# Performance work log

Measured on AMD Instinct MI355X. Metric: run time of the kernel, lower is better.

The kernel has to match this reference:

```python
import jax, jax.numpy as jnp
import numpy as np

HEADS = 8
HEAD_DIM = 32
PRE_H = 32
PRE_W = 32
SCALE = HEAD_DIM ** (-0.5)


def _relative_indices(H, W):
    # Faithful to torch loop: out[p, q] = (gy[q]-y_p+H)*W + (gx[q]-x_p+W)
    gy, gx = np.meshgrid(np.arange(H), np.arange(W), indexing='ij')
    gy = gy.reshape(-1)
    gx = gx.reshape(-1)
    idx = (gy[None, :] - gy[:, None] + H) * W + (gx[None, :] - gx[:, None] + W)
    return idx.astype(np.int32)  # [HW, HW]


def setup_inputs() -> dict:
    key = jax.random.key(0)
    ks = jax.random.split(key, 7)
    b, c, H, W = 16, 256, PRE_H, PRE_W
    dim = HEADS * HEAD_DIM  # 256
    x = jax.random.normal(ks[0], (b, c, H, W), dtype=jnp.float32)
    # nn.Linear weights: [out_features, in_features]
    Wq = jax.random.normal(ks[1], (dim, c), dtype=jnp.float32) * 0.02
    Wk = jax.random.normal(ks[2], (dim, c), dtype=jnp.float32) * 0.02
    Wv = jax.random.normal(ks[3], (dim, c), dtype=jnp.float32) * 0.02
    Wo = jax.random.normal(ks[4], (c, dim), dtype=jnp.float32) * 0.02
    bo = jax.random.normal(ks[5], (c,), dtype=jnp.float32) * 0.02
    rel_bias = jax.random.normal(ks[6], (HEADS, (2 * PRE_H - 1) * (2 * PRE_W - 1)), dtype=jnp.float32)
    rel_idx = jnp.asarray(_relative_indices(PRE_H, PRE_W))
    return {"x": x, "Wq": Wq, "Wk": Wk, "Wv": Wv, "Wo": Wo, "bo": bo,
            "rel_bias": rel_bias, "rel_idx": rel_idx}


def reference(x, Wq, Wk, Wv, Wo, bo, rel_bias, rel_idx):
    b, c, H, W = x.shape
    n = H * W
    h, d = HEADS, HEAD_DIM
    # b c h w -> b (h w) c
    xt = x.reshape(b, c, n).transpose(0, 2, 1)
    q = (xt @ Wq.T).reshape(b, n, h, d).transpose(0, 2, 1, 3)  # b h n d
    k = (xt @ Wk.T).reshape(b, n, h, d).transpose(0, 2, 1, 3)
    v = (xt @ Wv.T).reshape(b, n, h, d).transpose(0, 2, 1, 3)
    k = k * SCALE
    # gathered relative bias: [h, n, n]
    bias = rel_bias[:, rel_idx]
    attn = jnp.einsum('bhnd,bhmd->bhnm', q, k) + bias[None]
    attn = jax.nn.softmax(attn, axis=-1)
    out = jnp.einsum('bhnm,bhmd->bhnd', attn, v)
    out = out.transpose(0, 2, 1, 3).reshape(b, n, h * d)  # b n (h d)
    out = out @ Wo.T + bo
    # b (h w) c -> b c h w
    return out.transpose(0, 2, 1).reshape(b, c, H, W)
```

## Files before the change

kernel.cpp:

```cpp
#include <hip/hip_runtime.h>

#define HEADS 8
#define HDIM 32
#define NTOK 1024
#define CDIM 256
#define BATCH 16
#define ATT_SCALE 0.17677669529663687f
#define L2E 1.4426950408889634f
#define BSTR 1544

typedef __attribute__((ext_vector_type(8))) short bf16x8;
typedef __attribute__((ext_vector_type(4))) float f32x4;

__device__ __forceinline__ unsigned short f2bf(float f) {
    unsigned int u = __float_as_uint(f);
    return (unsigned short)((u + 0x7fffu + ((u >> 16) & 1u)) >> 16);
}

__device__ __forceinline__ unsigned cvt_pk_bf16(float lo, float hi) {
    unsigned r;
    asm("v_cvt_pk_bf16_f32 %0, %1, %2" : "=v"(r) : "v"(lo), "v"(hi));
    return r;
}

__global__ __launch_bounds__(256) void prep_kernel(
    const float* __restrict__ x,
    const float* __restrict__ Wq, const float* __restrict__ Wk,
    const float* __restrict__ Wv, const float* __restrict__ Wo,
    unsigned short* __restrict__ w16, unsigned short* __restrict__ xt16)
{
    const int t = threadIdx.x;
    if (blockIdx.z == 16) {
        const int which = blockIdx.y;
        const float* src = (which == 0) ? Wq : ((which == 1) ? Wk : ((which == 2) ? Wv : Wo));
        const float scale = (which == 1) ? (ATT_SCALE * L2E) : 1.0f;
        const int base = (blockIdx.x * 256 + t) * 16;
        #pragma unroll
        for (int i = 0; i < 4; ++i) {
            const int idx = base + i * 4;
            float4 v = *(const float4*)&src[idx];
            union { unsigned short h[4]; uint2 u; } pk;
            pk.h[0] = f2bf(v.x * scale); pk.h[1] = f2bf(v.y * scale);
            pk.h[2] = f2bf(v.z * scale); pk.h[3] = f2bf(v.w * scale);
            *(uint2*)&w16[(size_t)which * 65536 + idx] = pk.u;
        }
        return;
    }
    __shared__ float tile[64][65];
    const int b = blockIdx.z, ct = blockIdx.y * 64, nt = blockIdx.x * 64;
    const float* xb = x + ((size_t)b * CDIM + ct) * NTOK + nt;
    const int cc = t >> 4, n4 = (t & 15) * 4;
    #pragma unroll
    for (int i = 0; i < 4; ++i) {
        float4 v = *(const float4*)&xb[(size_t)(cc + 16 * i) * NTOK + n4];
        tile[cc + 16 * i][n4]     = v.x;
        tile[cc + 16 * i][n4 + 1] = v.y;
        tile[cc + 16 * i][n4 + 2] = v.z;
        tile[cc + 16 * i][n4 + 3] = v.w;
    }
    __syncthreads();
    const int c0 = (t & 7) * 8;
    #pragma unroll
    for (int i = 0; i < 2; ++i) {
        const int nl = (t >> 3) + 32 * i;
        union { unsigned short h[8]; uint4 u; } pk;
        #pragma unroll
        for (int j = 0; j < 8; ++j) pk.h[j] = f2bf(tile[c0 + j][nl]);
        *(uint4*)&xt16[((size_t)b * NTOK + nt + nl) * CDIM + ct + c0] = pk.u;
    }
}

__global__ __launch_bounds__(1024, 4) void attn_kernel(
    const unsigned short* __restrict__ xt16,
    const unsigned short* __restrict__ w16,
    const float* __restrict__ rel_bias,
    unsigned short* __restrict__ ao16)
{
    __shared__ __align__(16) unsigned char smem[65536 + 65536 + BSTR * 4 * 4];
    unsigned short* k_s   = (unsigned short*)smem;
    unsigned short* v_s   = (unsigned short*)(smem + 65536);
    unsigned short* q_s   = (unsigned short*)(smem + 65536);
    float*          bias4 = (float*)(smem + 131072);

    const int id   = blockIdx.x;
    const int bh_i = (id & 7) * 16 + (id >> 4);
    const int half = (id >> 3) & 1;
    const int b = bh_i >> 3, h = bh_i & 7;

    const int t = threadIdx.x, wid = t >> 6, lane = t & 63;
    const int g = lane >> 4, ln = lane & 15;
    const int qb = half * 512 + wid * 32;

    const unsigned short* xb  = xt16 + (size_t)b * NTOK * CDIM;
    const unsigned short* wqh = w16 + (size_t)(h * 32) * CDIM;
    const unsigned short* wkh = w16 + 65536 + (size_t)(h * 32) * CDIM;
    const unsigned short* wvh = w16 + 2 * 65536 + (size_t)(h * 32) * CDIM;

    {
        const int START = 544 - 512 * half;
        const float* brow = rel_bias + (size_t)h * 3969;
        for (int i = t; i < 1540; i += 1024) {
            #pragma unroll
            for (int a = 0; a < 4; ++a)
                bias4[a * BSTR + i] = brow[START + a + i] * L2E;
        }
    }

    bf16x8 aq0, aq1;
    {
        f32x4 acc[2][2];
        #pragma unroll
        for (int m = 0; m < 2; ++m)
            #pragma unroll
            for (int n = 0; n < 2; ++n) acc[m][n] = (f32x4){0.f, 0.f, 0.f, 0.f};
        #pragma unroll
        for (int kt = 0; kt < CDIM; kt += 32) {
            bf16x8 a[2], w2[2];
            #pragma unroll
            for (int m = 0; m < 2; ++m)
                a[m] = *(const bf16x8*)&xb[(size_t)(qb + m * 16 + ln) * CDIM + kt + g * 8];
            #pragma unroll
            for (int n = 0; n < 2; ++n)
                w2[n] = *(const bf16x8*)&wqh[(size_t)(n * 16 + ln) * CDIM + kt + g * 8];
            #pragma unroll
            for (int m = 0; m < 2; ++m)
                #pragma unroll
                for (int n = 0; n < 2; ++n)
                    acc[m][n] = __builtin_amdgcn_mfma_f32_16x16x32_bf16(a[m], w2[n], acc[m][n], 0, 0, 0);
        }
        const int lr = wid * 32;
        #pragma unroll
        for (int m = 0; m < 2; ++m)
            #pragma unroll
            for (int n = 0; n < 2; ++n)
                #pragma unroll
                for (int r = 0; r < 4; ++r)
                    q_s[(size_t)(lr + m * 16 + g * 4 + r) * HDIM + n * 16 + ln] = f2bf(acc[m][n][r]);
        aq0 = *(const bf16x8*)&q_s[(size_t)(lr + ln) * HDIM + g * 8];
        aq1 = *(const bf16x8*)&q_s[(size_t)(lr + 16 + ln) * HDIM + g * 8];
    }

    __syncthreads();

    {
        const int tr = wid * 64;
        f32x4 ak[4][2], av[2][4];
        #pragma unroll
        for (int m = 0; m < 4; ++m)
            #pragma unroll
            for (int n = 0; n < 2; ++n) {
                ak[m][n] = (f32x4){0.f, 0.f, 0.f, 0.f};
                av[n][m] = (f32x4){0.f, 0.f, 0.f, 0.f};
            }
        #pragma unroll
        for (int kt = 0; kt < CDIM; kt += 32) {
            bf16x8 xf[4], wkf[2], wvf[2];
            #pragma unroll
            for (int m = 0; m < 4; ++m)
                xf[m] = *(const bf16x8*)&xb[(size_t)(tr + m * 16 + ln) * CDIM + kt + g * 8];
            #pragma unroll
            for (int n = 0; n < 2; ++n) {
                wkf[n] = *(const bf16x8*)&wkh[(size_t)(n * 16 + ln) * CDIM + kt + g * 8];
                wvf[n] = *(const bf16x8*)&wvh[(size_t)(n * 16 + ln) * CDIM + kt + g * 8];
            }
            #pragma unroll
            for (int m = 0; m < 4; ++m) {
                ak[m][0] = __builtin_amdgcn_mfma_f32_16x16x32_bf16(xf[m], wkf[0], ak[m][0], 0, 0, 0);
                ak[m][1] = __builtin_amdgcn_mfma_f32_16x16x32_bf16(xf[m], wkf[1], ak[m][1], 0, 0, 0);
                av[0][m] = __builtin_amdgcn_mfma_f32_16x16x32_bf16(wvf[0], xf[m], av[0][m], 0, 0, 0);
                av[1][m] = __builtin_amdgcn_mfma_f32_16x16x32_bf16(wvf[1], xf[m], av[1][m], 0, 0, 0);
            }
        }
        #pragma unroll
        for (int m = 0; m < 4; ++m) {
            const int fbase = (2 * wid + (m >> 1)) * 2 + (g & 1);
            #pragma unroll
            for (int n = 0; n < 2; ++n) {
                const int lhi = (2 * n + (ln >> 3)) * 16 + ((m & 1) * 2 + (g >> 1)) * 4;
                #pragma unroll
                for (int r = 0; r < 4; ++r)
                    k_s[fbase * 512 + (lhi + r) * 8 + (ln & 7)] = f2bf(ak[m][n][r]);
            }
        }
        #pragma unroll
        for (int n = 0; n < 2; ++n)
            #pragma unroll
            for (int m = 0; m < 4; ++m) {
                const int fr  = (2 * wid + (m >> 1)) * 2 + n;
                const int lnb = ((m & 1) * 2 + (ln >> 3)) * 16 + g * 4;
                #pragma unroll
                for (int r = 0; r < 4; ++r)
                    v_s[fr * 512 + (lnb + r) * 8 + (ln & 7)] = f2bf(av[n][m][r]);
            }
    }

    __syncthreads();

    const int boffL = 512 + 8 * g - wid * 32 - ln;
    const int ba = boffL & 3;
    const float* bb = &bias4[ba * BSTR + (boffL - ba)];
    const unsigned short* kfp = k_s + lane * 8;
    const unsigned short* vfp = v_s + lane * 8;

    f32x4 o00 = {0.f,0.f,0.f,0.f}, o01 = {0.f,0.f,0.f,0.f};
    f32x4 o10 = {0.f,0.f,0.f,0.f}, o11 = {0.f,0.f,0.f,0.f};
    f32x4 ls0 = {0.f,0.f,0.f,0.f}, ls1 = {0.f,0.f,0.f,0.f};
    const short one_bf = (short)0x3F80;
    const bf16x8 ones = {one_bf,one_bf,one_bf,one_bf,one_bf,one_bf,one_bf,one_bf};

    bf16x8 kf0 = *(const bf16x8*)&kfp[0];
    bf16x8 kf1 = *(const bf16x8*)&kfp[512];
    f32x4  cA0 = *(const f32x4*)&bb[0];
    f32x4  cA1 = *(const f32x4*)&bb[4];
    f32x4  cB0 = *(const f32x4*)&bb[-16];
    f32x4  cB1 = *(const f32x4*)&bb[-12];

    for (int kb = 0; kb < NTOK; kb += 32) {
        const int fi = (kb >> 5) * 2;
        const bf16x8 vA0 = *(const bf16x8*)&vfp[fi * 512];
        const bf16x8 vA1 = *(const bf16x8*)&vfp[(fi + 1) * 512];
        const int kn = (kb + 32) & (NTOK - 1);
        const int fn = (kn >> 5) * 2;
        const bf16x8 nk0 = *(const bf16x8*)&kfp[fn * 512];
        const bf16x8 nk1 = *(const bf16x8*)&kfp[(fn + 1) * 512];
        const f32x4  nA0 = *(const f32x4*)&bb[kn];
        const f32x4  nA1 = *(const f32x4*)&bb[kn + 4];
        const f32x4  nB0 = *(const f32x4*)&bb[kn - 16];
        const f32x4  nB1 = *(const f32x4*)&bb[kn - 12];

        __builtin_amdgcn_s_setprio(1);
        f32x4 s00 = __builtin_amdgcn_mfma_f32_16x16x32_bf16(kf0, aq0, cA0, 0, 0, 0);
        f32x4 s01 = __builtin_amdgcn_mfma_f32_16x16x32_bf16(kf1, aq0, cA1, 0, 0, 0);
        f32x4 s10 = __builtin_amdgcn_mfma_f32_16x16x32_bf16(kf0, aq1, cB0, 0, 0, 0);
        f32x4 s11 = __builtin_amdgcn_mfma_f32_16x16x32_bf16(kf1, aq1, cB1, 0, 0, 0);
        __builtin_amdgcn_s_setprio(0);

        union { unsigned u4[4]; bf16x8 v; } ap0, ap1;
        ap0.u4[0] = cvt_pk_bf16(__builtin_amdgcn_exp2f(s00[0]), __builtin_amdgcn_exp2f(s00[1]));
        ap0.u4[1] = cvt_pk_bf16(__builtin_amdgcn_exp2f(s00[2]), __builtin_amdgcn_exp2f(s00[3]));
        ap0.u4[2] = cvt_pk_bf16(__builtin_amdgcn_exp2f(s01[0]), __builtin_amdgcn_exp2f(s01[1]));
        ap0.u4[3] = cvt_pk_bf16(__builtin_amdgcn_exp2f(s01[2]), __builtin_amdgcn_exp2f(s01[3]));
        ap1.u4[0] = cvt_pk_bf16(__builtin_amdgcn_exp2f(s10[0]), __builtin_amdgcn_exp2f(s10[1]));
        ap1.u4[1] = cvt_pk_bf16(__builtin_amdgcn_exp2f(s10[2]), __builtin_amdgcn_exp2f(s10[3]));
        ap1.u4[2] = cvt_pk_bf16(__builtin_amdgcn_exp2f(s11[0]), __builtin_amdgcn_exp2f(s11[1]));
        ap1.u4[3] = cvt_pk_bf16(__builtin_amdgcn_exp2f(s11[2]), __builtin_amdgcn_exp2f(s11[3]));

        __builtin_amdgcn_s_setprio(1);
        o00 = __builtin_amdgcn_mfma_f32_16x16x32_bf16(ap0.v, vA0, o00, 0, 0, 0);
        o01 = __builtin_amdgcn_mfma_f32_16x16x32_bf16(ap0.v, vA1, o01, 0, 0, 0);
        ls0 = __builtin_amdgcn_mfma_f32_16x16x32_bf16(ap0.v, ones, ls0, 0, 0, 0);
        o10 = __builtin_amdgcn_mfma_f32_16x16x32_bf16(ap1.v, vA0, o10, 0, 0, 0);
        o11 = __builtin_amdgcn_mfma_f32_16x16x32_bf16(ap1.v, vA1, o11, 0, 0, 0);
        ls1 = __builtin_amdgcn_mfma_f32_16x16x32_bf16(ap1.v, ones, ls1, 0, 0, 0);
        __builtin_amdgcn_s_setprio(0);

        kf0 = nk0; kf1 = nk1;
        cA0 = nA0; cA1 = nA1; cB0 = nB0; cB1 = nB1;
    }

    #pragma unroll
    for (int r = 0; r < 4; ++r) {
        float i0 = 1.f / ls0[r], i1 = 1.f / ls1[r];
        o00[r] *= i0; o01[r] *= i0;
        o10[r] *= i1; o11[r] *= i1;
    }

    __syncthreads();
    unsigned short (*otr)[32][40] = (unsigned short(*)[32][40])smem;
    #pragma unroll
    for (int r = 0; r < 4; ++r) {
        otr[wid][g * 4 + r][ln]           = f2bf(o00[r]);
        otr[wid][g * 4 + r][16 + ln]      = f2bf(o01[r]);
        otr[wid][16 + g * 4 + r][ln]      = f2bf(o10[r]);
        otr[wid][16 + g * 4 + r][16 + ln] = f2bf(o11[r]);
    }
    const int row = lane >> 1;
    const int ch  = (lane & 1) * 16;
    uint4 st0 = *(uint4*)&otr[wid][row][ch];
    uint4 st1 = *(uint4*)&otr[wid][row][ch + 8];
    unsigned short* dst = &ao16[((size_t)b * NTOK + qb + row) * CDIM + h * HDIM + ch];
    *(uint4*)dst     = st0;
    *(uint4*)&dst[8] = st1;
}

__global__ __launch_bounds__(256) void outproj_kernel(
    const unsigned short* __restrict__ ao16,
    const unsigned short* __restrict__ wo16,
    const float* __restrict__ bo,
    float* __restrict__ y)
{
    const int id   = blockIdx.x;
    const int b    = (id & 7) * 2 + ((id >> 3) & 1);
    const int rest = id >> 4;
    const int ct   = (rest & 3) * 64;
    const int pt   = (rest >> 2) * 128;
    const int t = threadIdx.x, wid = t >> 6, lane = t & 63;
    const int g = lane >> 4, ln = lane & 15;
    const int cb2 = ct + (wid & 1) * 32;
    const int pb  = pt + (wid >> 1) * 64;
    const unsigned short* ab = ao16 + (size_t)b * NTOK * CDIM;

    f32x4 acc[2][4];
    #pragma unroll
    for (int n = 0; n < 2; ++n)
        #pragma unroll
        for (int m = 0; m < 4; ++m) acc[n][m] = (f32x4){0.f, 0.f, 0.f, 0.f};

    #pragma unroll
    for (int kt = 0; kt < CDIM; kt += 32) {
        bf16x8 aw[2], bx[4];
        #pragma unroll
        for (int n = 0; n < 2; ++n)
            aw[n] = *(const bf16x8*)&wo16[(size_t)(cb2 + n * 16 + ln) * CDIM + kt + g * 8];
        #pragma unroll
        for (int m = 0; m < 4; ++m)
            bx[m] = *(const bf16x8*)&ab[(size_t)(pb + m * 16 + ln) * CDIM + kt + g * 8];
        #pragma unroll
        for (int n = 0; n < 2; ++n)
            #pragma unroll
            for (int m = 0; m < 4; ++m)
                acc[n][m] = __builtin_amdgcn_mfma_f32_16x16x32_bf16(aw[n], bx[m], acc[n][m], 0, 0, 0);
    }
    #pragma unroll
    for (int n = 0; n < 2; ++n)
        #pragma unroll
        for (int r = 0; r < 4; ++r) {
            const int c = cb2 + n * 16 + g * 4 + r;
            const float bias = bo[c];
            #pragma unroll
            for (int m = 0; m < 4; ++m)
                y[((size_t)b * CDIM + c) * NTOK + pb + m * 16 + ln] = acc[n][m][r] + bias;
        }
}

extern "C" void kernel_launch(void* const* d_in, const int* in_sizes, int n_in,
                              void* d_out, int out_size, void* d_ws, size_t ws_size,
                              hipStream_t stream) {
    const float* x        = (const float*)d_in[0];
    const float* Wq       = (const float*)d_in[1];
    const float* Wk       = (const float*)d_in[2];
    const float* Wv       = (const float*)d_in[3];
    const float* Wo       = (const float*)d_in[4];
    const float* bo       = (const float*)d_in[5];
    const float* rel_bias = (const float*)d_in[6];
    (void)in_sizes; (void)n_in; (void)ws_size; (void)out_size;

    unsigned short* ws16 = (unsigned short*)d_ws;
    unsigned short* xt16 = ws16;
    unsigned short* ao16 = ws16 + (size_t)4 * 1024 * 1024;
    unsigned short* w16  = ws16 + (size_t)8 * 1024 * 1024;
    float* y = (float*)d_out;

    prep_kernel<<<dim3(16, 4, 17), 256, 0, stream>>>(x, Wq, Wk, Wv, Wo, w16, xt16);
    attn_kernel<<<256, 1024, 0, stream>>>(xt16, w16, rel_bias, ao16);
    outproj_kernel<<<512, 256, 0, stream>>>(ao16, w16 + 3 * 65536, bo, y);
}
```

Before: 168.4 us.

## Fuse prep, attention and output projection into one cooperative persistent kernel

Merges the three kernels (bf16 conversion and transpose, attention, output projection) into a single cooperative kernel of 256 blocks of 1024 threads, separated by grid-wide syncs. This removes two kernel launch boundaries and the tail gaps between them. In exchange, the output projection and prep phases now run with the attention kernel's large shared-memory and register footprint and only 256 blocks. Grid syncs add their own barrier overhead and need every block to be co-resident.

```diff
diff --git a/kernel.cpp b/kernel.cpp
--- a/kernel.cpp
+++ b/kernel.cpp
@@ -1,4 +1,7 @@
 #include <hip/hip_runtime.h>
+#include <hip/hip_cooperative_groups.h>
+
+namespace cg = cooperative_groups;
 
 #define HEADS 8
 #define HDIM 32
@@ -23,314 +26,319 @@
     return r;
 }
 
-__global__ __launch_bounds__(256) void prep_kernel(
+__global__ __launch_bounds__(1024, 4) void fused_kernel(
     const float* __restrict__ x,
     const float* __restrict__ Wq, const float* __restrict__ Wk,
     const float* __restrict__ Wv, const float* __restrict__ Wo,
-    unsigned short* __restrict__ w16, unsigned short* __restrict__ xt16)
-{
-    const int t = threadIdx.x;
-    if (blockIdx.z == 16) {
-        const int which = blockIdx.y;
-        const float* src = (which == 0) ? Wq : ((which == 1) ? Wk : ((which == 2) ? Wv : Wo));
-        const float scale = (which == 1) ? (ATT_SCALE * L2E) : 1.0f;
-        const int base = (blockIdx.x * 256 + t) * 16;
-        #pragma unroll
-        for (int i = 0; i < 4; ++i) {
-            const int idx = base + i * 4;
-            float4 v = *(const float4*)&src[idx];
-            union { unsigned short h[4]; uint2 u; } pk;
-            pk.h[0] = f2bf(v.x * scale); pk.h[1] = f2bf(v.y * scale);
-            pk.h[2] = f2bf(v.z * scale); pk.h[3] = f2bf(v.w * scale);
-            *(uint2*)&w16[(size_t)which * 65536 + idx] = pk.u;
-        }
-        return;
-    }
-    __shared__ float tile[64][65];
-    const int b = blockIdx.z, ct = blockIdx.y * 64, nt = blockIdx.x * 64;
-    const float* xb = x + ((size_t)b * CDIM + ct) * NTOK + nt;
-    const int cc = t >> 4, n4 = (t & 15) * 4;
-    #pragma unroll
-    for (int i = 0; i < 4; ++i) {
-        float4 v = *(const float4*)&xb[(size_t)(cc + 16 * i) * NTOK + n4];
-        tile[cc + 16 * i][n4]     = v.x;
-        tile[cc + 16 * i][n4 + 1] = v.y;
-        tile[cc + 16 * i][n4 + 2] = v.z;
-        tile[cc + 16 * i][n4 + 3] = v.w;
-    }
-    __syncthreads();
-    const int c0 = (t & 7) * 8;
-    #pragma unroll
-    for (int i = 0; i < 2; ++i) {
-        const int nl = (t >> 3) + 32 * i;
-        union { unsigned short h[8]; uint4 u; } pk;
-        #pragma unroll
-        for (int j = 0; j < 8; ++j) pk.h[j] = f2bf(tile[c0 + j][nl]);
-        *(uint4*)&xt16[((size_t)b * NTOK + nt + nl) * CDIM + ct + c0] = pk.u;
-    }
-}
-
-__global__ __launch_bounds__(1024, 4) void attn_kernel(
-    const unsigned short* __restrict__ xt16,
-    const unsigned short* __restrict__ w16,
-    const float* __restrict__ rel_bias,
-    unsigned short* __restrict__ ao16)
+    const float* __restrict__ bo, const float* __restrict__ rel_bias,
+    unsigned short* __restrict__ w16, unsigned short* __restrict__ xt16,
+    unsigned short* __restrict__ ao16, float* __restrict__ y)
 {
     __shared__ __align__(16) unsigned char smem[65536 + 65536 + BSTR * 4 * 4];
-    unsigned short* k_s   = (unsigned short*)smem;
-    unsigned short* v_s   = (unsigned short*)(smem + 65536);
-    unsigned short* q_s   = (unsigned short*)(smem + 65536);
-    float*          bias4 = (float*)(smem + 131072);
-
-    const int id   = blockIdx.x;
-    const int bh_i = (id & 7) * 16 + (id >> 4);
-    const int half = (id >> 3) & 1;
-    const int b = bh_i >> 3, h = bh_i & 7;
-
-    const int t = threadIdx.x, wid = t >> 6, lane = t & 63;
-    const int g = lane >> 4, ln = lane & 15;
-    const int qb = half * 512 + wid * 32;
-
-    const unsigned short* xb  = xt16 + (size_t)b * NTOK * CDIM;
-    const unsigned short* wqh = w16 + (size_t)(h * 32) * CDIM;
-    const unsigned short* wkh = w16 + 65536 + (size_t)(h * 32) * CDIM;
-    const unsigned short* wvh = w16 + 2 * 65536 + (size_t)(h * 32) * CDIM;
+    const int t = threadIdx.x;
 
     {
-        const int START = 544 - 512 * half;
-        const float* brow = rel_bias + (size_t)h * 3969;
-        for (int i = t; i < 1540; i += 1024) {
-            #pragma unroll
-            for (int a = 0; a < 4; ++a)
-                bias4[a * BSTR + i] = brow[START + a + i] * L2E;
+        const int B = blockIdx.x;
+        float (*tile4)[64][65] = (float(*)[64][65])smem;
+        const int slot = t >> 8, tt = t & 255;
+        const int T = B * 4 + slot;
+        const int b1 = T >> 6;
+        const int ctf = ((T >> 4) & 3) * 64;
+        const int ntf = (T & 15) * 64;
+        const float* xb1 = x + ((size_t)b1 * CDIM + ctf) * NTOK + ntf;
+        const int cc = tt >> 4, n4 = (tt & 15) * 4;
+        #pragma unroll
+        for (int i = 0; i < 4; ++i) {
+            float4 v = *(const float4*)&xb1[(size_t)(cc + 16 * i) * NTOK + n4];
+            tile4[slot][cc + 16 * i][n4]     = v.x;
+            tile4[slot][cc + 16 * i][n4 + 1] = v.y;
+            tile4[slot][cc + 16 * i][n4 + 2] = v.z;
+            tile4[slot][cc + 16 * i][n4 + 3] = v.w;
+        }
+        if (B < 16) {
+            const int which = B & 3;
+            const float* src = (which == 0) ? Wq : ((which == 1) ? Wk : ((which == 2) ? Wv : Wo));
+            const float scale = (which == 1) ? (ATT_SCALE * L2E) : 1.0f;
+            const int base = ((B >> 2) * 1024 + t) * 16;
+            #pragma unroll
+            for (int i = 0; i < 4; ++i) {
+                const int idx = base + i * 4;
+                float4 v = *(const float4*)&src[idx];
+                union { unsigned short h[4]; uint2 u; } pk;
+                pk.h[0] = f2bf(v.x * scale); pk.h[1] = f2bf(v.y * scale);
+                pk.h[2] = f2bf(v.z * scale); pk.h[3] = f2bf(v.w * scale);
+                *(uint2*)&w16[(size_t)which * 65536 + idx] = pk.u;
+            }
+        }
+        __syncthreads();
+        const int c0 = (tt & 7) * 8;
+        #pragma unroll
+        for (int i = 0; i < 2; ++i) {
+            const int nl = (tt >> 3) + 32 * i;
+            union { unsigned short h[8]; uint4 u; } pk;
+            #pragma unroll
+            for (int j = 0; j < 8; ++j) pk.h[j] = f2bf(tile4[slot][c0 + j][nl]);
+            *(uint4*)&xt16[((size_t)b1 * NTOK + ntf + nl) * CDIM + ctf + c0] = pk.u;
         }
     }
 
-    bf16x8 aq0, aq1;
+    cg::this_grid().sync();
+
     {
+        unsigned short* k_s   = (unsigned short*)smem;
+        unsigned short* v_s   = (unsigned short*)(smem + 65536);
+        unsigned short* q_s   = (unsigned short*)(smem + 65536);
+        float*          bias4 = (float*)(smem + 131072);
+
+        const int id   = blockIdx.x;
+        const int bh_i = (id & 7) * 16 + (id >> 4);
+        const int half = (id >> 3) & 1;
+        const int b = bh_i >> 3, h = bh_i & 7;
+
+        const int wid = t >> 6, lane = t & 63;
+        const int g = lane >> 4, ln = lane & 15;
+        const int qb = half * 512 + wid * 32;
+
+        const unsigned short* xb  = xt16 + (size_t)b * NTOK * CDIM;
+        const unsigned short* wqh = w16 + (size_t)(h * 32) * CDIM;
+        const unsigned short* wkh = w16 + 65536 + (size_t)(h * 32) * CDIM;
+        const unsigned short* wvh = w16 + 2 * 65536 + (size_t)(h * 32) * CDIM;
+
+        {
+            const int START = 544 - 512 * half;
+            const float* brow = rel_bias + (size_t)h * 3969;
+            for (int i = t; i < 1540; i += 1024) {
+                #pragma unroll
+                for (int a = 0; a < 4; ++a)
+                    bias4[a * BSTR + i] = brow[START + a + i] * L2E;
+            }
+        }
+
+        bf16x8 aq0, aq1;
+        {
+            f32x4 acc[2][2];
+            #pragma unroll
+            for (int m = 0; m < 2; ++m)
+                #pragma unroll
+                for (int n = 0; n < 2; ++n) acc[m][n] = (f32x4){0.f, 0.f, 0.f, 0.f};
+            #pragma unroll
+            for (int kt = 0; kt < CDIM; kt += 32) {
+                bf16x8 a[2], w2[2];
+                #pragma unroll
+                for (int m = 0; m < 2; ++m)
+                    a[m] = *(const bf16x8*)&xb[(size_t)(qb + m * 16 + ln) * CDIM + kt + g * 8];
+                #pragma unroll
+                for (int n = 0; n < 2; ++n)
+                    w2[n] = *(const bf16x8*)&wqh[(size_t)(n * 16 + ln) * CDIM + kt + g * 8];
+                #pragma unroll
+                for (int m = 0; m < 2; ++m)
+                    #pragma unroll
+                    for (int n = 0; n < 2; ++n)
+                        acc[m][n] = __builtin_amdgcn_mfma_f32_16x16x32_bf16(a[m], w2[n], acc[m][n], 0, 0, 0);
+            }
+            const int lr = wid * 32;
+            #pragma unroll
+            for (int m = 0; m < 2; ++m)
+                #pragma unroll
+                for (int n = 0; n < 2; ++n)
+                    #pragma unroll
+                    for (int r = 0; r < 4; ++r)
+                        q_s[(size_t)(lr + m * 16 + g * 4 + r) * HDIM + n * 16 + ln] = f2bf(acc[m][n][r]);
+            aq0 = *(const bf16x8*)&q_s[(size_t)(lr + ln) * HDIM + g * 8];
+            aq1 = *(const bf16x8*)&q_s[(size_t)(lr + 16 + ln) * HDIM + g * 8];
+        }
+
+        __syncthreads();
+
+        {
+            const int tr = wid * 64;
+            f32x4 ak[4][2], av[2][4];
+            #pragma unroll
+            for (int m = 0; m < 4; ++m)
+                #pragma unroll
+                for (int n = 0; n < 2; ++n) {
+                    ak[m][n] = (f32x4){0.f, 0.f, 0.f, 0.f};
+                    av[n][m] = (f32x4){0.f, 0.f, 0.f, 0.f};
+                }
+            #pragma unroll
+            for (int kt = 0; kt < CDIM; kt += 32) {
+                bf16x8 xf[4], wkf[2], wvf[2];
+                #pragma unroll
+                for (int m = 0; m < 4; ++m)
+                    xf[m] = *(const bf16x8*)&xb[(size_t)(tr + m * 16 + ln) * CDIM + kt + g * 8];
+                #pragma unroll
+                for (int n = 0; n < 2; ++n) {
+                    wkf[n] = *(const bf16x8*)&wkh[(size_t)(n * 16 + ln) * CDIM + kt + g * 8];
+                    wvf[n] = *(const bf16x8*)&wvh[(size_t)(n * 16 + ln) * CDIM + kt + g * 8];
+                }
+                #pragma unroll
+                for (int m = 0; m < 4; ++m) {
+                    ak[m][0] = __builtin_amdgcn_mfma_f32_16x16x32_bf16(xf[m], wkf[0], ak[m][0], 0, 0, 0);
+                    ak[m][1] = __builtin_amdgcn_mfma_f32_16x16x32_bf16(xf[m], wkf[1], ak[m][1], 0, 0, 0);
+                    av[0][m] = __builtin_amdgcn_mfma_f32_16x16x32_bf16(wvf[0], xf[m], av[0][m], 0, 0, 0);
+                    av[1][m] = __builtin_amdgcn_mfma_f32_16x16x32_bf16(wvf[1], xf[m], av[1][m], 0, 0, 0);
+                }
+            }
+            #pragma unroll
+            for (int m = 0; m < 4; ++m) {
+                const int fbase = (2 * wid + (m >> 1)) * 2 + (g & 1);
+                #pragma unroll
+                for (int n = 0; n < 2; ++n) {
+                    const int lhi = (2 * n + (ln >> 3)) * 16 + ((m & 1) * 2 + (g >> 1)) * 4;
+                    #pragma unroll
+                    for (int r = 0; r < 4; ++r)
+                        k_s[fbase * 512 + (lhi + r) * 8 + (ln & 7)] = f2bf(ak[m][n][r]);
+                }
+            }
+            #pragma unroll
+            for (int n = 0; n < 2; ++n)
+                #pragma unroll
+                for (int m = 0; m < 4; ++m) {
+                    const int fr  = (2 * wid + (m >> 1)) * 2 + n;
+                    const int lnb = ((m & 1) * 2 + (ln >> 3)) * 16 + g * 4;
+                    #pragma unroll
+                    for (int r = 0; r < 4; ++r)
+                        v_s[fr * 512 + (lnb + r) * 8 + (ln & 7)] = f2bf(av[n][m][r]);
+                }
+        }
+
+        __syncthreads();
+
+        const int boffL = 512 + 8 * g - wid * 32 - ln;
+        const int ba = boffL & 3;
+        const float* bb = &bias4[ba * BSTR + (boffL - ba)];
+        const unsigned short* kfp = k_s + lane * 8;
+        const unsigned short* vfp = v_s + lane * 8;
+
+        f32x4 o00 = {0.f,0.f,0.f,0.f}, o01 = {0.f,0.f,0.f,0.f};
+        f32x4 o10 = {0.f,0.f,0.f,0.f}, o11 = {0.f,0.f,0.f,0.f};
+        f32x4 ls0 = {0.f,0.f,0.f,0.f}, ls1 = {0.f,0.f,0.f,0.f};
+        const short one_bf = (short)0x3F80;
+        const bf16x8 ones = {one_bf,one_bf,one_bf,one_bf,one_bf,one_bf,one_bf,one_bf};
+
+        bf16x8 kf0 = *(const bf16x8*)&kfp[0];
+        bf16x8 kf1 = *(const bf16x8*)&kfp[512];
+        f32x4  cA0 = *(const f32x4*)&bb[0];
+        f32x4  cA1 = *(const f32x4*)&bb[4];
+        f32x4  cB0 = *(const f32x4*)&bb[-16];
+        f32x4  cB1 = *(const f32x4*)&bb[-12];
+
+        for (int kb = 0; kb < NTOK; kb += 32) {
+            const int fi = (kb >> 5) * 2;
+            const bf16x8 vA0 = *(const bf16x8*)&vfp[fi * 512];
+            const bf16x8 vA1 = *(const bf16x8*)&vfp[(fi + 1) * 512];
+            const int kn = (kb + 32) & (NTOK - 1);
+            const int fn = (kn >> 5) * 2;
+            const bf16x8 nk0 = *(const bf16x8*)&kfp[fn * 512];
+            const bf16x8 nk1 = *(const bf16x8*)&kfp[(fn + 1) * 512];
+            const f32x4  nA0 = *(const f32x4*)&bb[kn];
+            const f32x4  nA1 = *(const f32x4*)&bb[kn + 4];
+            const f32x4  nB0 = *(const f32x4*)&bb[kn - 16];
+            const f32x4  nB1 = *(const f32x4*)&bb[kn - 12];
+
+            __builtin_amdgcn_s_setprio(1);
+            f32x4 s00 = __builtin_amdgcn_mfma_f32_16x16x32_bf16(kf0, aq0, cA0, 0, 0, 0);
+            f32x4 s01 = __builtin_amdgcn_mfma_f32_16x16x32_bf16(kf1, aq0, cA1, 0, 0, 0);
+            f32x4 s10 = __builtin_amdgcn_mfma_f32_16x16x32_bf16(kf0, aq1, cB0, 0, 0, 0);
+            f32x4 s11 = __builtin_amdgcn_mfma_f32_16x16x32_bf16(kf1, aq1, cB1, 0, 0, 0);
+            __builtin_amdgcn_s_setprio(0);
+
+            union { unsigned u4[4]; bf16x8 v; } ap0, ap1;
+            ap0.u4[0] = cvt_pk_bf16(__builtin_amdgcn_exp2f(s00[0]), __builtin_amdgcn_exp2f(s00[1]));
+            ap0.u4[1] = cvt_pk_bf16(__builtin_amdgcn_exp2f(s00[2]), __builtin_amdgcn_exp2f(s00[3]));
+            ap0.u4[2] = cvt_pk_bf16(__builtin_amdgcn_exp2f(s01[0]), __builtin_amdgcn_exp2f(s01[1]));
+            ap0.u4[3] = cvt_pk_bf16(__builtin_amdgcn_exp2f(s01[2]), __builtin_amdgcn_exp2f(s01[3]));
+            ap1.u4[0] = cvt_pk_bf16(__builtin_amdgcn_exp2f(s10[0]), __builtin_amdgcn_exp2f(s10[1]));
+            ap1.u4[1] = cvt_pk_bf16(__builtin_amdgcn_exp2f(s10[2]), __builtin_amdgcn_exp2f(s10[3]));
+            ap1.u4[2] = cvt_pk_bf16(__builtin_amdgcn_exp2f(s11[0]), __builtin_amdgcn_exp2f(s11[1]));
+            ap1.u4[3] = cvt_pk_bf16(__builtin_amdgcn_exp2f(s11[2]), __builtin_amdgcn_exp2f(s11[3]));
+
+            __builtin_amdgcn_s_setprio(1);
+            o00 = __builtin_amdgcn_mfma_f32_16x16x32_bf16(ap0.v, vA0, o00, 0, 0, 0);
+            o01 = __builtin_amdgcn_mfma_f32_16x16x32_bf16(ap0.v, vA1, o01, 0, 0, 0);
+            ls0 = __builtin_amdgcn_mfma_f32_16x16x32_bf16(ap0.v, ones, ls0, 0, 0, 0);
+            o10 = __builtin_amdgcn_mfma_f32_16x16x32_bf16(ap1.v, vA0, o10, 0, 0, 0);
+            o11 = __builtin_amdgcn_mfma_f32_16x16x32_bf16(ap1.v, vA1, o11, 0, 0, 0);
+            ls1 = __builtin_amdgcn_mfma_f32_16x16x32_bf16(ap1.v, ones, ls1, 0, 0, 0);
+            __builtin_amdgcn_s_setprio(0);
+
+            kf0 = nk0; kf1 = nk1;
+            cA0 = nA0; cA1 = nA1; cB0 = nB0; cB1 = nB1;
+        }
+
+        #pragma unroll
+        for (int r = 0; r < 4; ++r) {
+            float i0 = 1.f / ls0[r], i1 = 1.f / ls1[r];
+            o00[r] *= i0; o01[r] *= i0;
+            o10[r] *= i1; o11[r] *= i1;
+        }
+
+        __syncthreads();
+        unsigned short (*otr)[32][40] = (unsigned short(*)[32][40])smem;
+        #pragma unroll
+        for (int r = 0; r < 4; ++r) {
+            otr[wid][g * 4 + r][ln]           = f2bf(o00[r]);
+            otr[wid][g * 4 + r][16 + ln]      = f2bf(o01[r]);
+            otr[wid][16 + g * 4 + r][ln]      = f2bf(o10[r]);
+            otr[wid][16 + g * 4 + r][16 + ln] = f2bf(o11[r]);
+        }
+        const int row = lane >> 1;
+        const int ch  = (lane & 1) * 16;
+        uint4 st0 = *(uint4*)&otr[wid][row][ch];
+        uint4 st1 = *(uint4*)&otr[wid][row][ch + 8];
+        unsigned short* dst = &ao16[((size_t)b * NTOK + qb + row) * CDIM + h * HDIM + ch];
+        *(uint4*)dst     = st0;
+        *(uint4*)&dst[8] = st1;
+    }
+
+    cg::this_grid().sync();
+
+    {
+        const int t256 = t & 255, sub = t >> 8;
+        const int sid = blockIdx.x * 4 + sub;
+        const int b3   = (sid & 7) * 2 + ((sid >> 3) & 1);
+        const int rest = sid >> 4;
+        const int ct3 = (rest & 3) * 64;
+        const int pt3 = (rest >> 2) * 64;
+        const int wid3 = t256 >> 6, lane3 = t256 & 63;
+        const int g3 = lane3 >> 4, ln3 = lane3 & 15;
+        const int cb2 = ct3 + (wid3 & 1) * 32;
+        const int pb  = pt3 + (wid3 >> 1) * 32;
+        const unsigned short* ab   = ao16 + (size_t)b3 * NTOK * CDIM;
+        const unsigned short* wo16 = w16 + 3 * 65536;
+
         f32x4 acc[2][2];
         #pragma unroll
-        for (int m = 0; m < 2; ++m)
-            #pragma unroll
-            for (int n = 0; n < 2; ++n) acc[m][n] = (f32x4){0.f, 0.f, 0.f, 0.f};
+        for (int n = 0; n < 2; ++n)
+            #pragma unroll
+            for (int m = 0; m < 2; ++m) acc[n][m] = (f32x4){0.f, 0.f, 0.f, 0.f};
+
         #pragma unroll
         for (int kt = 0; kt < CDIM; kt += 32) {
-            bf16x8 a[2], w2[2];
+            bf16x8 aw[2], bx[2];
+            #pragma unroll
+            for (int n = 0; n < 2; ++n)
+                aw[n] = *(const bf16x8*)&wo16[(size_t)(cb2 + n * 16 + ln3) * CDIM + kt + g3 * 8];
             #pragma unroll
             for (int m = 0; m < 2; ++m)
-                a[m] = *(const bf16x8*)&xb[(size_t)(qb + m * 16 + ln) * CDIM + kt + g * 8];
+                bx[m] = *(const bf16x8*)&ab[(size_t)(pb + m * 16 + ln3) * CDIM + kt + g3 * 8];
             #pragma unroll
             for (int n = 0; n < 2; ++n)
-                w2[n] = *(const bf16x8*)&wqh[(size_t)(n * 16 + ln) * CDIM + kt + g * 8];
-            #pragma unroll
-            for (int m = 0; m < 2; ++m)
-                #pragma unroll
-                for (int n = 0; n < 2; ++n)
-                    acc[m][n] = __builtin_amdgcn_mfma_f32_16x16x32_bf16(a[m], w2[n], acc[m][n], 0, 0, 0);
-        }
-        const int lr = wid * 32;
-        #pragma unroll
-        for (int m = 0; m < 2; ++m)
-            #pragma unroll
-            for (int n = 0; n < 2; ++n)
-                #pragma unroll
-                for (int r = 0; r < 4; ++r)
-                    q_s[(size_t)(lr + m * 16 + g * 4 + r) * HDIM + n * 16 + ln] = f2bf(acc[m][n][r]);
-        aq0 = *(const bf16x8*)&q_s[(size_t)(lr + ln) * HDIM + g * 8];
-        aq1 = *(const bf16x8*)&q_s[(size_t)(lr + 16 + ln) * HDIM + g * 8];
+                #pragma unroll
+                for (int m = 0; m < 2; ++m)
+                    acc[n][m] = __builtin_amdgcn_mfma_f32_16x16x32_bf16(aw[n], bx[m], acc[n][m], 0, 0, 0);
+        }
+        #pragma unroll
+        for (int n = 0; n < 2; ++n)
+            #pragma unroll
+            for (int r = 0; r < 4; ++r) {
+                const int c = cb2 + n * 16 + g3 * 4 + r;
+                const float bias = bo[c];
+                #pragma unroll
+                for (int m = 0; m < 2; ++m)
+                    y[((size_t)b3 * CDIM + c) * NTOK + pb + m * 16 + ln3] = acc[n][m][r] + bias;
+            }
     }
-
-    __syncthreads();
-
-    {
-        const int tr = wid * 64;
-        f32x4 ak[4][2], av[2][4];
-        #pragma unroll
-        for (int m = 0; m < 4; ++m)
-            #pragma unroll
-            for (int n = 0; n < 2; ++n) {
-                ak[m][n] = (f32x4){0.f, 0.f, 0.f, 0.f};
-                av[n][m] = (f32x4){0.f, 0.f, 0.f, 0.f};
-            }
-        #pragma unroll
-        for (int kt = 0; kt < CDIM; kt += 32) {
-            bf16x8 xf[4], wkf[2], wvf[2];
-            #pragma unroll
-            for (int m = 0; m < 4; ++m)
-                xf[m] = *(const bf16x8*)&xb[(size_t)(tr + m * 16 + ln) * CDIM + kt + g * 8];
-            #pragma unroll
-            for (int n = 0; n < 2; ++n) {
-                wkf[n] = *(const bf16x8*)&wkh[(size_t)(n * 16 + ln) * CDIM + kt + g * 8];
-                wvf[n] = *(const bf16x8*)&wvh[(size_t)(n * 16 + ln) * CDIM + kt + g * 8];
-            }
-            #pragma unroll
-            for (int m = 0; m < 4; ++m) {
-                ak[m][0] = __builtin_amdgcn_mfma_f32_16x16x32_bf16(xf[m], wkf[0], ak[m][0], 0, 0, 0);
-                ak[m][1] = __builtin_amdgcn_mfma_f32_16x16x32_bf16(xf[m], wkf[1], ak[m][1], 0, 0, 0);
-                av[0][m] = __builtin_amdgcn_mfma_f32_16x16x32_bf16(wvf[0], xf[m], av[0][m], 0, 0, 0);
-                av[1][m] = __builtin_amdgcn_mfma_f32_16x16x32_bf16(wvf[1], xf[m], av[1][m], 0, 0, 0);
-            }
-        }
-        #pragma unroll
-        for (int m = 0; m < 4; ++m) {
-            const int fbase = (2 * wid + (m >> 1)) * 2 + (g & 1);
-            #pragma unroll
-            for (int n = 0; n < 2; ++n) {
-                const int lhi = (2 * n + (ln >> 3)) * 16 + ((m & 1) * 2 + (g >> 1)) * 4;
-                #pragma unroll
-                for (int r = 0; r < 4; ++r)
-                    k_s[fbase * 512 + (lhi + r) * 8 + (ln & 7)] = f2bf(ak[m][n][r]);
-            }
-        }
-        #pragma unroll
-        for (int n = 0; n < 2; ++n)
-            #pragma unroll
-            for (int m = 0; m < 4; ++m) {
-                const int fr  = (2 * wid + (m >> 1)) * 2 + n;
-                const int lnb = ((m & 1) * 2 + (ln >> 3)) * 16 + g * 4;
-                #pragma unroll
-                for (int r = 0; r < 4; ++r)
-                    v_s[fr * 512 + (lnb + r) * 8 + (ln & 7)] = f2bf(av[n][m][r]);
-            }
-    }
-
-    __syncthreads();
-
-    const int boffL = 512 + 8 * g - wid * 32 - ln;
-    const int ba = boffL & 3;
-    const float* bb = &bias4[ba * BSTR + (boffL - ba)];
-    const unsigned short* kfp = k_s + lane * 8;
-    const unsigned short* vfp = v_s + lane * 8;
-
-    f32x4 o00 = {0.f,0.f,0.f,0.f}, o01 = {0.f,0.f,0.f,0.f};
-    f32x4 o10 = {0.f,0.f,0.f,0.f}, o11 = {0.f,0.f,0.f,0.f};
-    f32x4 ls0 = {0.f,0.f,0.f,0.f}, ls1 = {0.f,0.f,0.f,0.f};
-    const short one_bf = (short)0x3F80;
-    const bf16x8 ones = {one_bf,one_bf,one_bf,one_bf,one_bf,one_bf,one_bf,one_bf};
-
-    bf16x8 kf0 = *(const bf16x8*)&kfp[0];
-    bf16x8 kf1 = *(const bf16x8*)&kfp[512];
-    f32x4  cA0 = *(const f32x4*)&bb[0];
-    f32x4  cA1 = *(const f32x4*)&bb[4];
-    f32x4  cB0 = *(const f32x4*)&bb[-16];
-    f32x4  cB1 = *(const f32x4*)&bb[-12];
-
-    for (int kb = 0; kb < NTOK; kb += 32) {
-        const int fi = (kb >> 5) * 2;
-        const bf16x8 vA0 = *(const bf16x8*)&vfp[fi * 512];
-        const bf16x8 vA1 = *(const bf16x8*)&vfp[(fi + 1) * 512];
-        const int kn = (kb + 32) & (NTOK - 1);
-        const int fn = (kn >> 5) * 2;
-        const bf16x8 nk0 = *(const bf16x8*)&kfp[fn * 512];
-        const bf16x8 nk1 = *(const bf16x8*)&kfp[(fn + 1) * 512];
-        const f32x4  nA0 = *(const f32x4*)&bb[kn];
-        const f32x4  nA1 = *(const f32x4*)&bb[kn + 4];
-        const f32x4  nB0 = *(const f32x4*)&bb[kn - 16];
-        const f32x4  nB1 = *(const f32x4*)&bb[kn - 12];
-
-        __builtin_amdgcn_s_setprio(1);
-        f32x4 s00 = __builtin_amdgcn_mfma_f32_16x16x32_bf16(kf0, aq0, cA0, 0, 0, 0);
-        f32x4 s01 = __builtin_amdgcn_mfma_f32_16x16x32_bf16(kf1, aq0, cA1, 0, 0, 0);
-        f32x4 s10 = __builtin_amdgcn_mfma_f32_16x16x32_bf16(kf0, aq1, cB0, 0, 0, 0);
-        f32x4 s11 = __builtin_amdgcn_mfma_f32_16x16x32_bf16(kf1, aq1, cB1, 0, 0, 0);
-        __builtin_amdgcn_s_setprio(0);
-
-        union { unsigned u4[4]; bf16x8 v; } ap0, ap1;
-        ap0.u4[0] = cvt_pk_bf16(__builtin_amdgcn_exp2f(s00[0]), __builtin_amdgcn_exp2f(s00[1]));
-        ap0.u4[1] = cvt_pk_bf16(__builtin_amdgcn_exp2f(s00[2]), __builtin_amdgcn_exp2f(s00[3]));
-        ap0.u4[2] = cvt_pk_bf16(__builtin_amdgcn_exp2f(s01[0]), __builtin_amdgcn_exp2f(s01[1]));
-        ap0.u4[3] = cvt_pk_bf16(__builtin_amdgcn_exp2f(s01[2]), __builtin_amdgcn_exp2f(s01[3]));
-        ap1.u4[0] = cvt_pk_bf16(__builtin_amdgcn_exp2f(s10[0]), __builtin_amdgcn_exp2f(s10[1]));
-        ap1.u4[1] = cvt_pk_bf16(__builtin_amdgcn_exp2f(s10[2]), __builtin_amdgcn_exp2f(s10[3]));
-        ap1.u4[2] = cvt_pk_bf16(__builtin_amdgcn_exp2f(s11[0]), __builtin_amdgcn_exp2f(s11[1]));
-        ap1.u4[3] = cvt_pk_bf16(__builtin_amdgcn_exp2f(s11[2]), __builtin_amdgcn_exp2f(s11[3]));
-
-        __builtin_amdgcn_s_setprio(1);
-        o00 = __builtin_amdgcn_mfma_f32_16x16x32_bf16(ap0.v, vA0, o00, 0, 0, 0);
-        o01 = __builtin_amdgcn_mfma_f32_16x16x32_bf16(ap0.v, vA1, o01, 0, 0, 0);
-        ls0 = __builtin_amdgcn_mfma_f32_16x16x32_bf16(ap0.v, ones, ls0, 0, 0, 0);
-        o10 = __builtin_amdgcn_mfma_f32_16x16x32_bf16(ap1.v, vA0, o10, 0, 0, 0);
-        o11 = __builtin_amdgcn_mfma_f32_16x16x32_bf16(ap1.v, vA1, o11, 0, 0, 0);
-        ls1 = __builtin_amdgcn_mfma_f32_16x16x32_bf16(ap1.v, ones, ls1, 0, 0, 0);
-        __builtin_amdgcn_s_setprio(0);
-
-        kf0 = nk0; kf1 = nk1;
-        cA0 = nA0; cA1 = nA1; cB0 = nB0; cB1 = nB1;
-    }
-
-    #pragma unroll
-    for (int r = 0; r < 4; ++r) {
-        float i0 = 1.f / ls0[r], i1 = 1.f / ls1[r];
-        o00[r] *= i0; o01[r] *= i0;
-        o10[r] *= i1; o11[r] *= i1;
-    }
-
-    __syncthreads();
-    unsigned short (*otr)[32][40] = (unsigned short(*)[32][40])smem;
-    #pragma unroll
-    for (int r = 0; r < 4; ++r) {
-        otr[wid][g * 4 + r][ln]           = f2bf(o00[r]);
-        otr[wid][g * 4 + r][16 + ln]      = f2bf(o01[r]);
-        otr[wid][16 + g * 4 + r][ln]      = f2bf(o10[r]);
-        otr[wid][16 + g * 4 + r][16 + ln] = f2bf(o11[r]);
-    }
-    const int row = lane >> 1;
-    const int ch  = (lane & 1) * 16;
-    uint4 st0 = *(uint4*)&otr[wid][row][ch];
-    uint4 st1 = *(uint4*)&otr[wid][row][ch + 8];
-    unsigned short* dst = &ao16[((size_t)b * NTOK + qb + row) * CDIM + h * HDIM + ch];
-    *(uint4*)dst     = st0;
-    *(uint4*)&dst[8] = st1;
-}
-
-__global__ __launch_bounds__(256) void outproj_kernel(
-    const unsigned short* __restrict__ ao16,
-    const unsigned short* __restrict__ wo16,
-    const float* __restrict__ bo,
-    float* __restrict__ y)
-{
-    const int id   = blockIdx.x;
-    const int b    = (id & 7) * 2 + ((id >> 3) & 1);
-    const int rest = id >> 4;
-    const int ct   = (rest & 3) * 64;
-    const int pt   = (rest >> 2) * 128;
-    const int t = threadIdx.x, wid = t >> 6, lane = t & 63;
-    const int g = lane >> 4, ln = lane & 15;
-    const int cb2 = ct + (wid & 1) * 32;
-    const int pb  = pt + (wid >> 1) * 64;
-    const unsigned short* ab = ao16 + (size_t)b * NTOK * CDIM;
-
-    f32x4 acc[2][4];
-    #pragma unroll
-    for (int n = 0; n < 2; ++n)
-        #pragma unroll
-        for (int m = 0; m < 4; ++m) acc[n][m] = (f32x4){0.f, 0.f, 0.f, 0.f};
-
-    #pragma unroll
-    for (int kt = 0; kt < CDIM; kt += 32) {
-        bf16x8 aw[2], bx[4];
-        #pragma unroll
-        for (int n = 0; n < 2; ++n)
-            aw[n] = *(const bf16x8*)&wo16[(size_t)(cb2 + n * 16 + ln) * CDIM + kt + g * 8];
-        #pragma unroll
-        for (int m = 0; m < 4; ++m)
-            bx[m] = *(const bf16x8*)&ab[(size_t)(pb + m * 16 + ln) * CDIM + kt + g * 8];
-        #pragma unroll
-        for (int n = 0; n < 2; ++n)
-            #pragma unroll
-            for (int m = 0; m < 4; ++m)
-                acc[n][m] = __builtin_amdgcn_mfma_f32_16x16x32_bf16(aw[n], bx[m], acc[n][m], 0, 0, 0);
-    }
-    #pragma unroll
-    for (int n = 0; n < 2; ++n)
-        #pragma unroll
-        for (int r = 0; r < 4; ++r) {
-            const int c = cb2 + n * 16 + g * 4 + r;
-            const float bias = bo[c];
-            #pragma unroll
-            for (int m = 0; m < 4; ++m)
-                y[((size_t)b * CDIM + c) * NTOK + pb + m * 16 + ln] = acc[n][m][r] + bias;
-        }
 }
 
 extern "C" void kernel_launch(void* const* d_in, const int* in_sizes, int n_in,
@@ -351,7 +359,11 @@
     unsigned short* w16  = ws16 + (size_t)8 * 1024 * 1024;
     float* y = (float*)d_out;
 
-    prep_kernel<<<dim3(16, 4, 17), 256, 0, stream>>>(x, Wq, Wk, Wv, Wo, w16, xt16);
-    attn_kernel<<<256, 1024, 0, stream>>>(xt16, w16, rel_bias, ao16);
-    outproj_kernel<<<512, 256, 0, stream>>>(ao16, w16 + 3 * 65536, bo, y);
+    void* args[] = {
+        (void*)&x, (void*)&Wq, (void*)&Wk, (void*)&Wv, (void*)&Wo,
+        (void*)&bo, (void*)&rel_bias, (void*)&w16, (void*)&xt16,
+        (void*)&ao16, (void*)&y
+    };
+    hipLaunchCooperativeKernel((void*)fused_kernel, dim3(256), dim3(1024),
+                               args, 0, stream);
 }
```

New measurement: 261.5 us. 1.55x slower.

## Split QKV projection into its own kernel to avoid redundant K/V compute

Applied to the files above, without the earlier changes.

Previously each attention block (one per batch, head and query-half) recomputed the K and V projections for all 1024 tokens, so that work was done twice per head. A new qkv_kernel computes Q, K and V once per token half and writes them to global workspace, already in the fragment layout the attention loop expects. The attention kernel then only loads the K/V fragments into shared memory and reads its Q fragments directly. This adds a kernel launch and a global write/read round trip of Q/K/V, and the workspace is reorganised so the attention output aliases the transposed-x buffer.

```diff
diff --git a/kernel.cpp b/kernel.cpp
--- a/kernel.cpp
+++ b/kernel.cpp
@@ -70,16 +70,103 @@
     }
 }
 
-__global__ __launch_bounds__(1024, 4) void attn_kernel(
+__global__ __launch_bounds__(1024, 4) void qkv_kernel(
     const unsigned short* __restrict__ xt16,
     const unsigned short* __restrict__ w16,
+    unsigned short* __restrict__ q16,
+    unsigned short* __restrict__ k16,
+    unsigned short* __restrict__ v16)
+{
+    const int id   = blockIdx.x;
+    const int bh_i = (id & 7) * 16 + (id >> 4);
+    const int tokhalf = (id >> 3) & 1;
+    const int b = bh_i >> 3, h = bh_i & 7;
+
+    const int t = threadIdx.x, wid = t >> 6, lane = t & 63;
+    const int g = lane >> 4, ln = lane & 15;
+    const int tr = tokhalf * 512 + wid * 32;
+
+    const unsigned short* xb  = xt16 + (size_t)b * NTOK * CDIM;
+    const unsigned short* wqh = w16 + (size_t)(h * 32) * CDIM;
+    const unsigned short* wkh = w16 + 65536 + (size_t)(h * 32) * CDIM;
+    const unsigned short* wvh = w16 + 2 * 65536 + (size_t)(h * 32) * CDIM;
+
+    f32x4 aq[2][2], ak[2][2], av[2][2];
+    #pragma unroll
+    for (int m = 0; m < 2; ++m)
+        #pragma unroll
+        for (int n = 0; n < 2; ++n) {
+            aq[m][n] = (f32x4){0.f, 0.f, 0.f, 0.f};
+            ak[m][n] = (f32x4){0.f, 0.f, 0.f, 0.f};
+            av[n][m] = (f32x4){0.f, 0.f, 0.f, 0.f};
+        }
+    #pragma unroll
+    for (int kt = 0; kt < CDIM; kt += 32) {
+        bf16x8 xf[2], wqf[2], wkf[2], wvf[2];
+        #pragma unroll
+        for (int m = 0; m < 2; ++m)
+            xf[m] = *(const bf16x8*)&xb[(size_t)(tr + m * 16 + ln) * CDIM + kt + g * 8];
+        #pragma unroll
+        for (int n = 0; n < 2; ++n) {
+            wqf[n] = *(const bf16x8*)&wqh[(size_t)(n * 16 + ln) * CDIM + kt + g * 8];
+            wkf[n] = *(const bf16x8*)&wkh[(size_t)(n * 16 + ln) * CDIM + kt + g * 8];
+            wvf[n] = *(const bf16x8*)&wvh[(size_t)(n * 16 + ln) * CDIM + kt + g * 8];
+        }
+        #pragma unroll
+        for (int m = 0; m < 2; ++m)
+            #pragma unroll
+            for (int n = 0; n < 2; ++n) {
+                aq[m][n] = __builtin_amdgcn_mfma_f32_16x16x32_bf16(xf[m], wqf[n], aq[m][n], 0, 0, 0);
+                ak[m][n] = __builtin_amdgcn_mfma_f32_16x16x32_bf16(xf[m], wkf[n], ak[m][n], 0, 0, 0);
+                av[n][m] = __builtin_amdgcn_mfma_f32_16x16x32_bf16(wvf[n], xf[m], av[n][m], 0, 0, 0);
+            }
+    }
+
+    #pragma unroll
+    for (int m = 0; m < 2; ++m)
+        #pragma unroll
+        for (int n = 0; n < 2; ++n)
+            #pragma unroll
+            for (int r = 0; r < 4; ++r)
+                q16[((size_t)(b * NTOK + tr + m * 16 + g * 4 + r) * 8 + h) * 32 + n * 16 + ln] =
+                    f2bf(aq[m][n][r]);
+
+    unsigned short* kb16 = k16 + (size_t)(b * 8 + h) * 32768;
+    const int fK = (tokhalf * 16 + wid) * 2 + (g & 1);
+    #pragma unroll
+    for (int m = 0; m < 2; ++m)
+        #pragma unroll
+        for (int n = 0; n < 2; ++n) {
+            const int lhi = (2 * n + (ln >> 3)) * 16 + (m * 2 + (g >> 1)) * 4;
+            #pragma unroll
+            for (int r = 0; r < 4; ++r)
+                kb16[fK * 512 + (lhi + r) * 8 + (ln & 7)] = f2bf(ak[m][n][r]);
+        }
+
+    unsigned short* vb16 = v16 + (size_t)(b * 8 + h) * 32768;
+    #pragma unroll
+    for (int n = 0; n < 2; ++n) {
+        const int fV = (tokhalf * 16 + wid) * 2 + n;
+        #pragma unroll
+        for (int m = 0; m < 2; ++m) {
+            const int lnb = (m * 2 + (ln >> 3)) * 16 + g * 4;
+            #pragma unroll
+            for (int r = 0; r < 4; ++r)
+                vb16[fV * 512 + (lnb + r) * 8 + (ln & 7)] = f2bf(av[n][m][r]);
+        }
+    }
+}
+
+__global__ __launch_bounds__(1024, 4) void attn_kernel(
+    const unsigned short* __restrict__ q16,
+    const unsigned short* __restrict__ k16,
+    const unsigned short* __restrict__ v16,
     const float* __restrict__ rel_bias,
     unsigned short* __restrict__ ao16)
 {
     __shared__ __align__(16) unsigned char smem[65536 + 65536 + BSTR * 4 * 4];
     unsigned short* k_s   = (unsigned short*)smem;
     unsigned short* v_s   = (unsigned short*)(smem + 65536);
-    unsigned short* q_s   = (unsigned short*)(smem + 65536);
     float*          bias4 = (float*)(smem + 131072);
 
     const int id   = blockIdx.x;
@@ -91,10 +178,18 @@
     const int g = lane >> 4, ln = lane & 15;
     const int qb = half * 512 + wid * 32;
 
-    const unsigned short* xb  = xt16 + (size_t)b * NTOK * CDIM;
-    const unsigned short* wqh = w16 + (size_t)(h * 32) * CDIM;
-    const unsigned short* wkh = w16 + 65536 + (size_t)(h * 32) * CDIM;
-    const unsigned short* wvh = w16 + 2 * 65536 + (size_t)(h * 32) * CDIM;
+    const unsigned short* kbh = k16 + (size_t)(b * 8 + h) * 32768;
+    const unsigned short* vbh = v16 + (size_t)(b * 8 + h) * 32768;
+
+    bf16x8 sk[4], sv[4];
+    #pragma unroll
+    for (int j = 0; j < 4; ++j) {
+        const int f = wid * 4 + j;
+        sk[j] = *(const bf16x8*)&kbh[(size_t)f * 512 + lane * 8];
+        sv[j] = *(const bf16x8*)&vbh[(size_t)f * 512 + lane * 8];
+    }
+    const bf16x8 aq0 = *(const bf16x8*)&q16[((size_t)(b * NTOK + qb + ln) * 8 + h) * 32 + g * 8];
+    const bf16x8 aq1 = *(const bf16x8*)&q16[((size_t)(b * NTOK + qb + 16 + ln) * 8 + h) * 32 + g * 8];
 
     {
         const int START = 544 - 512 * half;
@@ -106,92 +201,11 @@
         }
     }
 
-    bf16x8 aq0, aq1;
-    {
-        f32x4 acc[2][2];
-        #pragma unroll
-        for (int m = 0; m < 2; ++m)
-            #pragma unroll
-            for (int n = 0; n < 2; ++n) acc[m][n] = (f32x4){0.f, 0.f, 0.f, 0.f};
-        #pragma unroll
-        for (int kt = 0; kt < CDIM; kt += 32) {
-            bf16x8 a[2], w2[2];
-            #pragma unroll
-            for (int m = 0; m < 2; ++m)
-                a[m] = *(const bf16x8*)&xb[(size_t)(qb + m * 16 + ln) * CDIM + kt + g * 8];
-            #pragma unroll
-            for (int n = 0; n < 2; ++n)
-                w2[n] = *(const bf16x8*)&wqh[(size_t)(n * 16 + ln) * CDIM + kt + g * 8];
-            #pragma unroll
-            for (int m = 0; m < 2; ++m)
-                #pragma unroll
-                for (int n = 0; n < 2; ++n)
-                    acc[m][n] = __builtin_amdgcn_mfma_f32_16x16x32_bf16(a[m], w2[n], acc[m][n], 0, 0, 0);
-        }
-        const int lr = wid * 32;
-        #pragma unroll
-        for (int m = 0; m < 2; ++m)
-            #pragma unroll
-            for (int n = 0; n < 2; ++n)
-                #pragma unroll
-                for (int r = 0; r < 4; ++r)
-                    q_s[(size_t)(lr + m * 16 + g * 4 + r) * HDIM + n * 16 + ln] = f2bf(acc[m][n][r]);
-        aq0 = *(const bf16x8*)&q_s[(size_t)(lr + ln) * HDIM + g * 8];
-        aq1 = *(const bf16x8*)&q_s[(size_t)(lr + 16 + ln) * HDIM + g * 8];
-    }
-
-    __syncthreads();
-
-    {
-        const int tr = wid * 64;
-        f32x4 ak[4][2], av[2][4];
-        #pragma unroll
-        for (int m = 0; m < 4; ++m)
-            #pragma unroll
-            for (int n = 0; n < 2; ++n) {
-                ak[m][n] = (f32x4){0.f, 0.f, 0.f, 0.f};
-                av[n][m] = (f32x4){0.f, 0.f, 0.f, 0.f};
-            }
-        #pragma unroll
-        for (int kt = 0; kt < CDIM; kt += 32) {
-            bf16x8 xf[4], wkf[2], wvf[2];
-            #pragma unroll
-            for (int m = 0; m < 4; ++m)
-                xf[m] = *(const bf16x8*)&xb[(size_t)(tr + m * 16 + ln) * CDIM + kt + g * 8];
-            #pragma unroll
-            for (int n = 0; n < 2; ++n) {
-                wkf[n] = *(const bf16x8*)&wkh[(size_t)(n * 16 + ln) * CDIM + kt + g * 8];
-                wvf[n] = *(const bf16x8*)&wvh[(size_t)(n * 16 + ln) * CDIM + kt + g * 8];
-            }
-            #pragma unroll
-            for (int m = 0; m < 4; ++m) {
-                ak[m][0] = __builtin_amdgcn_mfma_f32_16x16x32_bf16(xf[m], wkf[0], ak[m][0], 0, 0, 0);
-                ak[m][1] = __builtin_amdgcn_mfma_f32_16x16x32_bf16(xf[m], wkf[1], ak[m][1], 0, 0, 0);
-                av[0][m] = __builtin_amdgcn_mfma_f32_16x16x32_bf16(wvf[0], xf[m], av[0][m], 0, 0, 0);
-                av[1][m] = __builtin_amdgcn_mfma_f32_16x16x32_bf16(wvf[1], xf[m], av[1][m], 0, 0, 0);
-            }
-        }
-        #pragma unroll
-        for (int m = 0; m < 4; ++m) {
-            const int fbase = (2 * wid + (m >> 1)) * 2 + (g & 1);
-            #pragma unroll
-            for (int n = 0; n < 2; ++n) {
-                const int lhi = (2 * n + (ln >> 3)) * 16 + ((m & 1) * 2 + (g >> 1)) * 4;
-                #pragma unroll
-                for (int r = 0; r < 4; ++r)
-                    k_s[fbase * 512 + (lhi + r) * 8 + (ln & 7)] = f2bf(ak[m][n][r]);
-            }
-        }
-        #pragma unroll
-        for (int n = 0; n < 2; ++n)
-            #pragma unroll
-            for (int m = 0; m < 4; ++m) {
-                const int fr  = (2 * wid + (m >> 1)) * 2 + n;
-                const int lnb = ((m & 1) * 2 + (ln >> 3)) * 16 + g * 4;
-                #pragma unroll
-                for (int r = 0; r < 4; ++r)
-                    v_s[fr * 512 + (lnb + r) * 8 + (ln & 7)] = f2bf(av[n][m][r]);
-            }
+    #pragma unroll
+    for (int j = 0; j < 4; ++j) {
+        const int f = wid * 4 + j;
+        *(bf16x8*)&k_s[(size_t)f * 512 + lane * 8] = sk[j];
+        *(bf16x8*)&v_s[(size_t)f * 512 + lane * 8] = sv[j];
     }
 
     __syncthreads();
@@ -347,11 +361,15 @@
 
     unsigned short* ws16 = (unsigned short*)d_ws;
     unsigned short* xt16 = ws16;
-    unsigned short* ao16 = ws16 + (size_t)4 * 1024 * 1024;
-    unsigned short* w16  = ws16 + (size_t)8 * 1024 * 1024;
+    unsigned short* ao16 = ws16;
+    unsigned short* w16  = ws16 + (size_t)4 * 1024 * 1024;
+    unsigned short* q16  = w16 + 4 * 65536;
+    unsigned short* k16  = q16 + (size_t)4 * 1024 * 1024;
+    unsigned short* v16  = k16 + (size_t)4 * 1024 * 1024;
     float* y = (float*)d_out;
 
     prep_kernel<<<dim3(16, 4, 17), 256, 0, stream>>>(x, Wq, Wk, Wv, Wo, w16, xt16);
-    attn_kernel<<<256, 1024, 0, stream>>>(xt16, w16, rel_bias, ao16);
+    qkv_kernel<<<256, 1024, 0, stream>>>(xt16, w16, q16, k16, v16);
+    attn_kernel<<<256, 1024, 0, stream>>>(q16, k16, v16, rel_bias, ao16);
     outproj_kernel<<<512, 256, 0, stream>>>(ao16, w16 + 3 * 65536, bo, y);
 }
```

Result: faster. 158.0 us (-6.2%).
